# Optimization experiments

Hardware: AMD Instinct MI355X
Metric: run time of the kernel (lower is better)

Reference implementation:

```python
import jax, jax.numpy as jnp
import numpy as np

LIDAR_MAX_X = 32.0
LIDAR_MAX_Y = 32.0


def bilinear_grid_sample(value, grid):
    """torch.nn.functional.grid_sample, mode='bilinear', padding_mode='zeros',
    align_corners=False.
    value: (B, C, H, W); grid: (B, Q, P, 2) in [-1, 1] (x=width, y=height).
    Returns (B, C, Q, P)."""
    B, C, H, W = value.shape
    x = (grid[..., 0] + 1.0) * (W / 2) - 0.5  # (B,Q,P) unnormalized col
    y = (grid[..., 1] + 1.0) * (H / 2) - 0.5  # (B,Q,P) unnormalized row
    x0 = jnp.floor(x)
    y0 = jnp.floor(y)
    x1 = x0 + 1.0
    y1 = y0 + 1.0
    wx1 = x - x0
    wx0 = 1.0 - wx1
    wy1 = y - y0
    wy0 = 1.0 - wy1
    vflat = value.reshape(B, C, H * W)

    def gather(ix, iy):
        valid = (ix >= 0) & (ix <= W - 1) & (iy >= 0) & (iy <= H - 1)
        ixc = jnp.clip(ix, 0, W - 1).astype(jnp.int32)
        iyc = jnp.clip(iy, 0, H - 1).astype(jnp.int32)
        idx = iyc * W + ixc  # (B,Q,P)
        g = jax.vmap(lambda v, i: v[:, i])(vflat, idx)  # (B,C,Q,P)
        return g * valid[:, None, :, :].astype(value.dtype)

    out = (gather(x0, y0) * (wx0 * wy0)[:, None]
           + gather(x1, y0) * (wx1 * wy0)[:, None]
           + gather(x0, y1) * (wx0 * wy1)[:, None]
           + gather(x1, y1) * (wx1 * wy1)[:, None])
    return out


def setup_inputs() -> dict:
    key = jax.random.key(0)
    ks = jax.random.split(key, 10)
    bs, Q, P, D = 16, 1024, 8, 256
    Cin, H, W = 64, 128, 128
    queries = jax.random.normal(ks[0], (bs, Q, D), dtype=jnp.float32)
    # scale so trajectory points span the +/-32m BEV extent
    traj_points = jax.random.normal(ks[1], (bs, Q, P, 2), dtype=jnp.float32) * 20.0
    bev_feature = jax.random.normal(ks[2], (bs, Cin, H, W), dtype=jnp.float32)
    spatial_shape = jnp.array([H, W], dtype=jnp.int64)
    attn_w = jax.random.normal(ks[3], (P, D), dtype=jnp.float32) * 0.02
    attn_b = jnp.zeros((P,), dtype=jnp.float32)
    conv_w = jax.random.normal(ks[4], (256, Cin, 3, 3), dtype=jnp.float32) * 0.05
    conv_b = jnp.zeros((256,), dtype=jnp.float32)
    out_w = jax.random.normal(ks[5], (D, D), dtype=jnp.float32) * (1.0 / np.sqrt(D))
    out_b = jnp.zeros((D,), dtype=jnp.float32)
    return {"queries": queries, "traj_points": traj_points,
            "bev_feature": bev_feature, "spatial_shape": spatial_shape,
            "attn_w": attn_w, "attn_b": attn_b,
            "conv_w": conv_w, "conv_b": conv_b,
            "out_w": out_w, "out_b": out_b}


def reference(queries, traj_points, bev_feature, spatial_shape,
              attn_w, attn_b, conv_w, conv_b, out_w, out_b):
    # normalize trajectory to [-1,1] and swap (y,x) -> (x,y) grid order
    grid = jnp.stack([traj_points[..., 1] / LIDAR_MAX_X,
                      traj_points[..., 0] / LIDAR_MAX_Y], axis=-1)  # (bs,Q,P,2)
    # per-query attention over the P sampled points
    attn = jax.nn.softmax(
        jnp.einsum('bqd,pd->bqp', queries, attn_w) + attn_b, axis=-1)  # (bs,Q,P)
    # value projection: 3x3 conv + ReLU
    value = jax.lax.conv_general_dilated(
        bev_feature, conv_w, window_strides=(1, 1),
        padding=((1, 1), (1, 1)),
        dimension_numbers=('NCHW', 'OIHW', 'NCHW'))
    value = jax.nn.relu(value + conv_b[None, :, None, None])  # (bs,256,H,W)
    sampled = bilinear_grid_sample(value, grid)  # (bs,256,Q,P)
    out = jnp.einsum('bcqp,bqp->bqc', sampled, attn)  # weighted sum + permute
    out = jnp.einsum('bqc,dc->bqd', out, out_w) + out_b
    # dropout is identity in eval mode
    return out + queries
```

## Files before the change

### kernel.cpp

```cpp
#include <hip/hip_runtime.h>
#include <stdint.h>


typedef __attribute__((ext_vector_type(8))) short short8;
typedef __attribute__((ext_vector_type(4))) float f32x4;

__device__ __forceinline__ unsigned short f2bf(float f) {
  union { float f; unsigned int u; } v; v.f = f;
  unsigned int r = (v.u + 0x7FFFu + ((v.u >> 16) & 1u)) >> 16;
  return (unsigned short)r;
}
__device__ __forceinline__ float bf2f(unsigned short h) {
  union { unsigned int u; float f; } v; v.u = ((unsigned int)h) << 16;
  return v.f;
}

__device__ __forceinline__ void gload_lds16(const void* g, void* l) {
  __builtin_amdgcn_global_load_lds(
      (const __attribute__((address_space(1))) unsigned int*)g,
      (__attribute__((address_space(3))) unsigned int*)l, 16, 0, 0);
}

__global__ __launch_bounds__(256) void k1_transpose(const float* __restrict__ bev,
                                                    unsigned short* __restrict__ nhwc) {
  __shared__ __align__(16) float lds[64 * 32 * 4];
  const int b = blockIdx.x >> 7, y = blockIdx.x & 127;
  const int t = threadIdx.x;
  const float* src = bev + (size_t)(b * 64) * 16384 + y * 128;
#pragma unroll
  for (int k = 0; k < 8; ++k) {
    int chunk = k * 256 + t;
    int ic = chunk >> 5, xq = chunk & 31;
    float4 v = *(const float4*)(src + ic * 16384 + xq * 4);
    int slot = xq ^ (ic >> 3);
    *(float4*)&lds[(ic * 32 + slot) * 4] = v;
  }
  __syncthreads();
  unsigned short* dst = nhwc + (size_t)blockIdx.x * 8192;
#pragma unroll
  for (int k = 0; k < 4; ++k) {
    int co = k * 256 + t;
    int x = co >> 3, icg = co & 7;
    int slot = (x >> 2) ^ icg;
    int w = x & 3;
    uint4 u;
    unsigned int* up = (unsigned int*)&u;
#pragma unroll
    for (int jj = 0; jj < 4; ++jj) {
      float v0 = lds[((icg * 8 + 2 * jj) * 32 + slot) * 4 + w];
      float v1 = lds[((icg * 8 + 2 * jj + 1) * 32 + slot) * 4 + w];
      up[jj] = (unsigned int)f2bf(v0) | ((unsigned int)f2bf(v1) << 16);
    }
    *(uint4*)(dst + x * 64 + icg * 8) = u;
  }
}

__global__ __launch_bounds__(256) void k1b_pack(const float* __restrict__ conv_w,
                                                const float* __restrict__ out_w,
                                                unsigned short* __restrict__ wconv,
                                                unsigned short* __restrict__ wout,
                                                float* __restrict__ zp) {
  const int tid = blockIdx.x * 256 + threadIdx.x;
  for (int idx = tid; idx < 9 * 8 * 256 * 8; idx += 16384) {
    int j = idx & 7, oc = (idx >> 3) & 255, g = (idx >> 11) & 7, o = idx >> 14;
    wconv[idx] = f2bf(conv_w[(oc * 64 + g * 8 + j) * 9 + o]);
  }
  for (int idx = tid; idx < 32 * 256 * 8; idx += 16384) {
    int j = idx & 7, d = (idx >> 3) & 255, g = idx >> 11;
    wout[idx] = f2bf(out_w[d * 256 + g * 8 + j]);
  }
  if (tid < 64) zp[tid] = 0.0f;
}

#define K2_LOADA(s, A) do {                                                   \
    _Pragma("unroll")                                                         \
    for (int ocf_ = 0; ocf_ < 4; ++ocf_)                                      \
      A[ocf_] = gA[(4 * (s) + g) * 256 + wo * 64 + ocf_ * 16 + l15];          \
  } while (0)

#define K2_READB(s, h, B) do {                                                \
    const int o_ = (s) >> 1, ich_ = (s) & 1;                                  \
    const int dyr_ = o_ / 3, dx_ = o_ - dyr_ * 3 - 1;                         \
    _Pragma("unroll")                                                         \
    for (int pf_ = 0; pf_ < 4; ++pf_)                                         \
      B[pf_] = lin[((rh + dyr_) * 8 + ich_ * 4 + g) * 130 + 1 + dx_ +         \
                   ((h) * 4 + pf_) * 16 + l15];                               \
  } while (0)

#define K2_MF(A, B, h) do {                                                   \
    _Pragma("unroll")                                                         \
    for (int ocf_ = 0; ocf_ < 4; ++ocf_)                                      \
      _Pragma("unroll")                                                       \
      for (int pf_ = 0; pf_ < 4; ++pf_)                                       \
        acc[ocf_][(h) * 4 + pf_] = __builtin_amdgcn_mfma_f32_16x16x32_bf16(   \
            A[ocf_], B[pf_], acc[ocf_][(h) * 4 + pf_], 0, 0, 0);              \
  } while (0)

__global__ __launch_bounds__(512, 2) void k2_conv(const unsigned short* __restrict__ nhwc,
                                                  const unsigned short* __restrict__ wconv,
                                                  const float* __restrict__ conv_b,
                                                  const float* __restrict__ zp,
                                                  unsigned short* __restrict__ value) {
  __shared__ __align__(16) char smem[66560];
  const short8* lin = (const short8*)smem;
  const short8* gA = (const short8*)wconv;
  const int bid = blockIdx.x;
  const int swz = (bid & 7) * 128 + (bid >> 3);
  const int b = swz >> 6, yp = swz & 63;
  const int y0 = yp * 2;
  const int t = threadIdx.x, wid = t >> 6, lane = t & 63;
  const int wo = wid >> 1, rh = wid & 1;
  const int g = lane >> 4, l15 = lane & 15;

  const unsigned short* bevb = nhwc + (size_t)b * (128 * 128 * 64);
  for (int i = wid; i < 65; i += 8) {
    const int chunk = i * 64 + lane;
    const int ridx = chunk / 1040;
    const int rem = chunk - ridx * 1040;
    const int icg = rem / 130;
    const int c = rem - icg * 130;
    const int yy = y0 - 1 + ridx, xx = c - 1;
    const void* src = (yy >= 0 && yy < 128 && xx >= 0 && xx < 128)
                          ? (const void*)(bevb + ((yy * 128 + xx) * 64 + icg * 8))
                          : (const void*)zp;
    gload_lds16(src, smem + i * 1024);
  }
  __syncthreads();

  const f32x4 z4 = {0.f, 0.f, 0.f, 0.f};
  f32x4 acc[4][8];
#pragma unroll
  for (int i = 0; i < 4; ++i)
#pragma unroll
    for (int j = 0; j < 8; ++j) acc[i][j] = z4;

  short8 A0[4], A1[4], B0[4], B1[4];
  K2_LOADA(0, A0);
  K2_LOADA(1, A1);

#pragma unroll
  for (int s = 0; s < 18; ++s) {
    K2_READB(s, 0, B0);
    K2_READB(s, 1, B1);
    if (s & 1) {
      K2_MF(A1, B0, 0);
      K2_MF(A1, B1, 1);
      if (s + 2 < 18) K2_LOADA(s + 2, A1);
    } else {
      K2_MF(A0, B0, 0);
      K2_MF(A0, B1, 1);
      if (s + 2 < 18) K2_LOADA(s + 2, A0);
    }
  }

  const int y = y0 + rh;
  unsigned short* vrow = value + (((size_t)(b * 128 + y) * 128 + l15) * 256);
#pragma unroll
  for (int ocf = 0; ocf < 4; ++ocf) {
    const int ocb = wo * 64 + ocf * 16 + g * 4;
    const float4 cb4 = *(const float4*)(conv_b + ocb);
#pragma unroll
    for (int pf = 0; pf < 8; ++pf) {
      ushort4 ov;
      float v0 = acc[ocf][pf][0] + cb4.x; ov.x = f2bf(v0 > 0.f ? v0 : 0.f);
      float v1 = acc[ocf][pf][1] + cb4.y; ov.y = f2bf(v1 > 0.f ? v1 : 0.f);
      float v2 = acc[ocf][pf][2] + cb4.z; ov.z = f2bf(v2 > 0.f ? v2 : 0.f);
      float v3 = acc[ocf][pf][3] + cb4.w; ov.w = f2bf(v3 > 0.f ? v3 : 0.f);
      *(ushort4*)(vrow + (size_t)pf * 16 * 256 + ocb) = ov;
    }
  }
}

__global__ __launch_bounds__(256) void k3_sample(const float* __restrict__ queries,
                                                 const float* __restrict__ traj,
                                                 const float* __restrict__ attn_w,
                                                 const float* __restrict__ attn_b,
                                                 const unsigned short* __restrict__ value,
                                                 unsigned short* __restrict__ S) {
  const int wid = threadIdx.x >> 6, lane = threadIdx.x & 63;
  const int qg = blockIdx.x * 4 + wid;
  const int b = qg >> 10;
  const float4 qv = ((const float4*)queries)[qg * 64 + lane];
  float a[8];
#pragma unroll
  for (int p = 0; p < 8; ++p) {
    float4 wv = ((const float4*)attn_w)[p * 64 + lane];
    float d = qv.x * wv.x + qv.y * wv.y + qv.z * wv.z + qv.w * wv.w;
#pragma unroll
    for (int off = 32; off >= 1; off >>= 1) d += __shfl_xor(d, off);
    a[p] = d + attn_b[p];
  }
  float mx = a[0];
#pragma unroll
  for (int p = 1; p < 8; ++p) mx = fmaxf(mx, a[p]);
  float ssum = 0.f;
#pragma unroll
  for (int p = 0; p < 8; ++p) { a[p] = __expf(a[p] - mx); ssum += a[p]; }
  const float inv = 1.f / ssum;

  float acc0 = 0.f, acc1 = 0.f, acc2 = 0.f, acc3 = 0.f;
  const unsigned short* vb = value + (size_t)b * (128 * 128 * 256);
  const int coff = lane * 4;
#pragma unroll
  for (int p = 0; p < 8; ++p) {
    const float ty = traj[(qg * 8 + p) * 2 + 0];
    const float tx = traj[(qg * 8 + p) * 2 + 1];
    const float fx = (tx * 0.03125f + 1.f) * 64.f - 0.5f;
    const float fy = (ty * 0.03125f + 1.f) * 64.f - 0.5f;
    const float fx0 = floorf(fx), fy0 = floorf(fy);
    const int ix0 = (int)fx0, iy0 = (int)fy0;
    const float wx1 = fx - fx0, wx0 = 1.f - wx1;
    const float wy1 = fy - fy0, wy0 = 1.f - wy1;
    const float ap = a[p] * inv;
    const float cw[4] = {wx0 * wy0 * ap, wx1 * wy0 * ap, wx0 * wy1 * ap, wx1 * wy1 * ap};
    const int cx[4] = {ix0, ix0 + 1, ix0, ix0 + 1};
    const int cy[4] = {iy0, iy0, iy0 + 1, iy0 + 1};
#pragma unroll
    for (int cc = 0; cc < 4; ++cc) {
      if (cx[cc] >= 0 && cx[cc] < 128 && cy[cc] >= 0 && cy[cc] < 128) {
        const ushort4 v = *(const ushort4*)(vb + (cy[cc] * 128 + cx[cc]) * 256 + coff);
        acc0 += cw[cc] * bf2f(v.x);
        acc1 += cw[cc] * bf2f(v.y);
        acc2 += cw[cc] * bf2f(v.z);
        acc3 += cw[cc] * bf2f(v.w);
      }
    }
  }
  ushort4 o;
  o.x = f2bf(acc0); o.y = f2bf(acc1); o.z = f2bf(acc2); o.w = f2bf(acc3);
  *(ushort4*)(S + (size_t)qg * 256 + coff) = o;
}

__global__ __launch_bounds__(256, 2) void k4_proj(const unsigned short* __restrict__ S,
                                                  const unsigned short* __restrict__ wout,
                                                  const float* __restrict__ out_b,
                                                  const float* __restrict__ queries,
                                                  float* __restrict__ out) {
  __shared__ __align__(16) char smem[8192];
  const short8* lds8 = (const short8*)smem;
  const short8* wp8 = (const short8*)wout;
  const int t = threadIdx.x, wid = t >> 6, lane = t & 63;
  const int q0 = blockIdx.x * 64;
  const int g = lane >> 4, l15 = lane & 15;
  const f32x4 z4 = {0.f, 0.f, 0.f, 0.f};
  f32x4 acc[4][4];
#pragma unroll
  for (int i = 0; i < 4; ++i)
#pragma unroll
    for (int j = 0; j < 4; ++j) acc[i][j] = z4;

  gload_lds16(S + ((size_t)(q0 + lane) * 256 + wid * 8), smem + wid * 1024);
  __syncthreads();

#pragma unroll
  for (int ks = 0; ks < 8; ++ks) {
    if (ks < 7)
      gload_lds16(S + ((size_t)(q0 + lane) * 256 + (ks + 1) * 32 + wid * 8),
                  smem + (((ks + 1) & 1) ? 4096 : 0) + wid * 1024);
    short8 af[4];
#pragma unroll
    for (int df = 0; df < 4; ++df)
      af[df] = wp8[(ks * 4 + g) * 256 + wid * 64 + df * 16 + l15];
    short8 bf[4];
    const short8* sb = lds8 + ((ks & 1) ? 256 : 0);
#pragma unroll
    for (int qf = 0; qf < 4; ++qf) bf[qf] = sb[g * 64 + qf * 16 + l15];
#pragma unroll
    for (int df = 0; df < 4; ++df)
#pragma unroll
      for (int qf = 0; qf < 4; ++qf)
        acc[df][qf] = __builtin_amdgcn_mfma_f32_16x16x32_bf16(af[df], bf[qf], acc[df][qf], 0, 0, 0);
    __syncthreads();
  }

#pragma unroll
  for (int df = 0; df < 4; ++df) {
    const int db = wid * 64 + df * 16 + g * 4;
    const float4 ob4 = *(const float4*)(out_b + db);
#pragma unroll
    for (int qf = 0; qf < 4; ++qf) {
      const int q = q0 + qf * 16 + l15;
      const float4 qv = *(const float4*)(queries + (size_t)q * 256 + db);
      float4 ov;
      ov.x = acc[df][qf][0] + ob4.x + qv.x;
      ov.y = acc[df][qf][1] + ob4.y + qv.y;
      ov.z = acc[df][qf][2] + ob4.z + qv.z;
      ov.w = acc[df][qf][3] + ob4.w + qv.w;
      *(float4*)(out + (size_t)q * 256 + db) = ov;
    }
  }
}

extern "C" void kernel_launch(void* const* d_in, const int* in_sizes, int n_in,
                              void* d_out, int out_size, void* d_ws, size_t ws_size,
                              hipStream_t stream) {
  const float* queries = (const float*)d_in[0];
  const float* traj    = (const float*)d_in[1];
  const float* bev     = (const float*)d_in[2];
  const float* attn_w  = (const float*)d_in[4];
  const float* attn_b  = (const float*)d_in[5];
  const float* conv_w  = (const float*)d_in[6];
  const float* conv_b  = (const float*)d_in[7];
  const float* out_w   = (const float*)d_in[8];
  const float* out_b   = (const float*)d_in[9];
  float* out = (float*)d_out;

  char* ws = (char*)d_ws;
  unsigned short* bev_nhwc = (unsigned short*)(ws);
  unsigned short* value    = (unsigned short*)(ws + 33554432);
  unsigned short* wconv    = (unsigned short*)(ws + 167772160);
  unsigned short* wout     = (unsigned short*)(ws + 168067072);
  unsigned short* Sbuf     = (unsigned short*)(ws + 168198144);
  float*          zp       = (float*)(ws + 176586752);

  k1_transpose<<<2048, 256, 0, stream>>>(bev, bev_nhwc);
  k1b_pack<<<64, 256, 0, stream>>>(conv_w, out_w, wconv, wout, zp);
  k2_conv<<<1024, 512, 0, stream>>>(bev_nhwc, wconv, conv_b, zp, value);
  k3_sample<<<4096, 256, 0, stream>>>(queries, traj, attn_w, attn_b, value, Sbuf);
  k4_proj<<<256, 256, 0, stream>>>(Sbuf, wout, out_b, queries, out);
}
```

Measured before the change: 160.4 us.

## Shrink conv blocks to one output row with four waves

```diff
diff --git a/kernel.cpp b/kernel.cpp
--- a/kernel.cpp
+++ b/kernel.cpp
@@ -83,7 +83,7 @@
     const int dyr_ = o_ / 3, dx_ = o_ - dyr_ * 3 - 1;                         \
     _Pragma("unroll")                                                         \
     for (int pf_ = 0; pf_ < 4; ++pf_)                                         \
-      B[pf_] = lin[((rh + dyr_) * 8 + ich_ * 4 + g) * 130 + 1 + dx_ +         \
+      B[pf_] = lin[(dyr_ * 8 + ich_ * 4 + g) * 130 + 1 + dx_ +                \
                    ((h) * 4 + pf_) * 16 + l15];                               \
   } while (0)
 
@@ -96,33 +96,34 @@
             A[ocf_], B[pf_], acc[ocf_][(h) * 4 + pf_], 0, 0, 0);              \
   } while (0)
 
-__global__ __launch_bounds__(512, 2) void k2_conv(const unsigned short* __restrict__ nhwc,
+__global__ __launch_bounds__(256, 2) void k2_conv(const unsigned short* __restrict__ nhwc,
                                                   const unsigned short* __restrict__ wconv,
                                                   const float* __restrict__ conv_b,
                                                   const float* __restrict__ zp,
                                                   unsigned short* __restrict__ value) {
-  __shared__ __align__(16) char smem[66560];
+  __shared__ __align__(16) char smem[50176];
   const short8* lin = (const short8*)smem;
   const short8* gA = (const short8*)wconv;
   const int bid = blockIdx.x;
-  const int swz = (bid & 7) * 128 + (bid >> 3);
-  const int b = swz >> 6, yp = swz & 63;
-  const int y0 = yp * 2;
+  const int swz = (bid & 7) * 256 + (bid >> 3);
+  const int b = swz >> 7, y = swz & 127;
   const int t = threadIdx.x, wid = t >> 6, lane = t & 63;
-  const int wo = wid >> 1, rh = wid & 1;
+  const int wo = wid;
   const int g = lane >> 4, l15 = lane & 15;
 
   const unsigned short* bevb = nhwc + (size_t)b * (128 * 128 * 64);
-  for (int i = wid; i < 65; i += 8) {
+  for (int i = wid; i < 49; i += 4) {
     const int chunk = i * 64 + lane;
-    const int ridx = chunk / 1040;
-    const int rem = chunk - ridx * 1040;
-    const int icg = rem / 130;
-    const int c = rem - icg * 130;
-    const int yy = y0 - 1 + ridx, xx = c - 1;
-    const void* src = (yy >= 0 && yy < 128 && xx >= 0 && xx < 128)
-                          ? (const void*)(bevb + ((yy * 128 + xx) * 64 + icg * 8))
-                          : (const void*)zp;
+    const void* src = (const void*)zp;
+    if (chunk < 3120) {
+      const int ridx = chunk / 1040;
+      const int rem = chunk - ridx * 1040;
+      const int icg = rem / 130;
+      const int c = rem - icg * 130;
+      const int yy = y - 1 + ridx, xx = c - 1;
+      if (yy >= 0 && yy < 128 && xx >= 0 && xx < 128)
+        src = (const void*)(bevb + ((yy * 128 + xx) * 64 + icg * 8));
+    }
     gload_lds16(src, smem + i * 1024);
   }
   __syncthreads();
@@ -153,19 +154,21 @@
     }
   }
 
-  const int y = y0 + rh;
   unsigned short* vrow = value + (((size_t)(b * 128 + y) * 128 + l15) * 256);
-#pragma unroll
-  for (int ocf = 0; ocf < 4; ++ocf) {
-    const int ocb = wo * 64 + ocf * 16 + g * 4;
-    const float4 cb4 = *(const float4*)(conv_b + ocb);
-#pragma unroll
-    for (int pf = 0; pf < 8; ++pf) {
+  float4 cb4[4];
+#pragma unroll
+  for (int ocf = 0; ocf < 4; ++ocf)
+    cb4[ocf] = *(const float4*)(conv_b + wo * 64 + ocf * 16 + g * 4);
+#pragma unroll
+  for (int pf = 0; pf < 8; ++pf) {
+#pragma unroll
+    for (int ocf = 0; ocf < 4; ++ocf) {
+      const int ocb = wo * 64 + ocf * 16 + g * 4;
       ushort4 ov;
-      float v0 = acc[ocf][pf][0] + cb4.x; ov.x = f2bf(v0 > 0.f ? v0 : 0.f);
-      float v1 = acc[ocf][pf][1] + cb4.y; ov.y = f2bf(v1 > 0.f ? v1 : 0.f);
-      float v2 = acc[ocf][pf][2] + cb4.z; ov.z = f2bf(v2 > 0.f ? v2 : 0.f);
-      float v3 = acc[ocf][pf][3] + cb4.w; ov.w = f2bf(v3 > 0.f ? v3 : 0.f);
+      float v0 = acc[ocf][pf][0] + cb4[ocf].x; ov.x = f2bf(v0 > 0.f ? v0 : 0.f);
+      float v1 = acc[ocf][pf][1] + cb4[ocf].y; ov.y = f2bf(v1 > 0.f ? v1 : 0.f);
+      float v2 = acc[ocf][pf][2] + cb4[ocf].z; ov.z = f2bf(v2 > 0.f ? v2 : 0.f);
+      float v3 = acc[ocf][pf][3] + cb4[ocf].w; ov.w = f2bf(v3 > 0.f ? v3 : 0.f);
       *(ushort4*)(vrow + (size_t)pf * 16 * 256 + ocb) = ov;
     }
   }
@@ -315,7 +318,7 @@
 
   k1_transpose<<<2048, 256, 0, stream>>>(bev, bev_nhwc);
   k1b_pack<<<64, 256, 0, stream>>>(conv_w, out_w, wconv, wout, zp);
-  k2_conv<<<1024, 512, 0, stream>>>(bev_nhwc, wconv, conv_b, zp, value);
+  k2_conv<<<2048, 256, 0, stream>>>(bev_nhwc, wconv, conv_b, zp, value);
   k3_sample<<<4096, 256, 0, stream>>>(queries, traj, attn_w, attn_b, value, Sbuf);
   k4_proj<<<256, 256, 0, stream>>>(Sbuf, wout, out_b, queries, out);
 }
```

Measured after the change: 158.2 us. Within noise of the previous version (-1.4%).
